# Kernel optimization log

Hardware: AMD Instinct MI355X
Metric: run time of the kernel (lower is better)

## Reference

```python
import jax, jax.numpy as jnp
import numpy as np

B, T, E = 2048, 200, 128
H1, H2 = 64, 32
NEG_INF = -(2.0 ** 32) + 1.0  # matches tf source's -2**32 + 1 padding value


def setup_inputs() -> dict:
    key = jax.random.key(0)
    ks = jax.random.split(key, 8)
    queries = jax.random.normal(ks[0], (B, E), dtype=jnp.float32)
    keys = jax.random.normal(ks[1], (B, T, E), dtype=jnp.float32)
    keys_id = jax.random.randint(ks[2], (B, T), 0, 2, dtype=jnp.int32)
    # Dense params: MLP input is concat([q,k,q-k,q*k]) -> 4*E = 512
    W1 = jax.random.normal(ks[3], (4 * E, H1), dtype=jnp.float32) * (1.0 / np.sqrt(4 * E))
    b1 = jnp.zeros((H1,), dtype=jnp.float32)
    W2 = jax.random.normal(ks[4], (H1, H2), dtype=jnp.float32) * (1.0 / np.sqrt(H1))
    b2 = jnp.zeros((H2,), dtype=jnp.float32)
    W3 = jax.random.normal(ks[5], (H2, 1), dtype=jnp.float32) * (1.0 / np.sqrt(H2))
    b3 = jnp.zeros((1,), dtype=jnp.float32)
    return {"queries": queries, "keys": keys, "keys_id": keys_id,
            "W1": W1, "b1": b1, "W2": W2, "b2": b2, "W3": W3, "b3": b3}


def reference(queries, keys, keys_id, W1, b1, W2, b2, W3, b3):
    # tile query over the time axis: [B,E] -> [B,T,E]
    q = jnp.broadcast_to(queries[:, None, :], keys.shape)
    # concat features: [B,T,4E]
    feat = jnp.concatenate([q, keys, q - keys, q * keys], axis=2)
    # small MLP scorer
    h = jax.nn.relu(jnp.einsum('btf,fh->bth', feat, W1) + b1)
    h = jax.nn.relu(jnp.einsum('bth,hk->btk', h, W2) + b2)
    weight = jnp.einsum('btk,ko->bto', h, W3) + b3  # [B,T,1]
    # masked softmax over time axis (padding id == 0)
    mask = (keys_id != 0)[:, :, None]  # [B,T,1]
    weight = jnp.where(mask, weight, jnp.float32(NEG_INF))
    weight = jax.nn.softmax(weight, axis=1)
    # weighted mean pooling (original uses reduce_mean, i.e. sum/T)
    return jnp.mean(weight * keys, axis=1)  # [B,E]
```

## Files before the change

kernel.cpp:

```cpp
#include <hip/hip_runtime.h>
#include <hip/hip_bf16.h>

#define NEG_INF_F (-4294967295.0f)

typedef __attribute__((ext_vector_type(8))) short bf16x8;
typedef __attribute__((ext_vector_type(4))) float f32x4;

__device__ __forceinline__ unsigned short f2bf(float x) {
    unsigned u = __float_as_uint(x);
    return (unsigned short)((u + 0x7fffu + ((u >> 16) & 1u)) >> 16);
}
__device__ __forceinline__ unsigned f2bf2(float a, float b) {
    __hip_bfloat162 h2 = __float22bfloat162_rn(make_float2(a, b));
    unsigned r; __builtin_memcpy(&r, &h2, 4); return r;
}
union FragU { unsigned u[4]; bf16x8 h; };

struct __align__(16) Smem {
    unsigned short Mt[64 * 128];
    unsigned short h1s[4][16 * 64];
    float q[128];
    float cpart[256];
    float Om[4][128];
    float mw[4], lw[4];
};

__global__ __launch_bounds__(256, 3)
void attn_fused(const float* __restrict__ Q,
                const float* __restrict__ Kg,
                const int*   __restrict__ kid,
                const float* __restrict__ W1,
                const float* __restrict__ b1,
                const float* __restrict__ W2,
                const float* __restrict__ b2,
                const float* __restrict__ W3,
                const float* __restrict__ b3,
                float* __restrict__ out)
{
    __shared__ Smem sm;
    const int b    = blockIdx.x;
    const int tid  = threadIdx.x;
    const int wave = tid >> 6;
    const int lane = tid & 63;
    const int l15  = lane & 15;
    const int quad = lane >> 4;

    if (tid < 128) sm.q[tid] = Q[b * 128 + tid];

    bf16x8 W2f[2][2];
    #pragma unroll
    for (int ks = 0; ks < 2; ++ks) {
        #pragma unroll
        for (int nt = 0; nt < 2; ++nt) {
            const int n = nt * 16 + l15;
            const int kb = ks * 32 + quad * 8;
            bf16x8 f;
            #pragma unroll
            for (int j = 0; j < 8; ++j) f[j] = (short)f2bf(W2[(kb + j) * 32 + n]);
            W2f[ks][nt] = f;
        }
    }
    const float w3a = W3[l15],  w3b = W3[16 + l15];
    const float b2a = b2[l15],  b2b = b2[16 + l15];
    const float b3v = b3[0];
    __syncthreads();

    {
        const int n  = tid & 63;
        const int ko = (tid >> 6) * 2;
        #pragma unroll
        for (int i = 0; i < 16; ++i) {
            const int k = i * 8 + ko;
            const float v0 = (W1[(128 + k) * 64 + n] - W1[(256 + k) * 64 + n])
                           + sm.q[k] * W1[(384 + k) * 64 + n];
            const float v1 = (W1[(129 + k) * 64 + n] - W1[(257 + k) * 64 + n])
                           + sm.q[k + 1] * W1[(385 + k) * 64 + n];
            const int g = (k >> 3) ^ (n & 15);
            *reinterpret_cast<unsigned*>(&sm.Mt[n * 128 + g * 8 + (k & 7)]) = f2bf2(v0, v1);
        }
    }
    {
        const int n = tid & 63, kc = tid >> 6;
        float acc = (kc == 0) ? b1[n] : 0.0f;
        #pragma unroll 4
        for (int i = 0; i < 32; ++i) {
            const int k = kc * 32 + i;
            acc += sm.q[k] * (W1[k * 64 + n] + W1[(256 + k) * 64 + n]);
        }
        sm.cpart[kc * 64 + n] = acc;
    }
    __syncthreads();

    float cn[4];
    #pragma unroll
    for (int nt = 0; nt < 4; ++nt) {
        const int n = nt * 16 + l15;
        cn[nt] = sm.cpart[n] + sm.cpart[64 + n] + sm.cpart[128 + n] + sm.cpart[192 + n];
    }

    const float* kbase = Kg + (size_t)b * 25600;
    unsigned short* h1w = &sm.h1s[wave][0];
    const f32x4 zero4 = {0.f, 0.f, 0.f, 0.f};

    float O[32];
    #pragma unroll
    for (int i = 0; i < 32; ++i) O[i] = 0.0f;
    float mrun = -__builtin_inff(), lrun = 0.0f;

    for (int tile = wave; tile < 13; tile += 4) {
        const int t0 = tile * 16;
        const int t  = t0 + l15;
        const int tr = min(t, 199);
        const float* kr = kbase + tr * 128;
        float4 ka[4], kb_[4];
        #pragma unroll
        for (int ks = 0; ks < 4; ++ks) {
            ka[ks]  = *reinterpret_cast<const float4*>(kr + ks * 32 + quad * 8);
            kb_[ks] = *reinterpret_cast<const float4*>(kr + ks * 32 + quad * 8 + 4);
        }
        const int kidv = kid[b * 200 + tr];

        f32x4 acc[4] = {zero4, zero4, zero4, zero4};
        #pragma unroll
        for (int ks = 0; ks < 4; ++ks) {
            FragU A;
            A.u[0] = f2bf2(ka[ks].x,  ka[ks].y);
            A.u[1] = f2bf2(ka[ks].z,  ka[ks].w);
            A.u[2] = f2bf2(kb_[ks].x, kb_[ks].y);
            A.u[3] = f2bf2(kb_[ks].z, kb_[ks].w);
            #pragma unroll
            for (int nt = 0; nt < 4; ++nt) {
                const int n = nt * 16 + l15;
                const int g = (ks * 4 + quad) ^ l15;
                const bf16x8 Bf = *reinterpret_cast<const bf16x8*>(&sm.Mt[n * 128 + g * 8]);
                acc[nt] = __builtin_amdgcn_mfma_f32_16x16x32_bf16(A.h, Bf, acc[nt], 0, 0, 0);
            }
        }
        #pragma unroll
        for (int nt = 0; nt < 4; ++nt) {
            const int n = nt * 16 + l15;
            #pragma unroll
            for (int r = 0; r < 4; ++r) {
                const int m = quad * 4 + r;
                const float h = fmaxf(acc[nt][r] + cn[nt], 0.0f);
                const int g = (n >> 3) ^ (m & 7);
                h1w[m * 64 + g * 8 + (n & 7)] = f2bf(h);
            }
        }
        f32x4 p0 = zero4, p1 = zero4;
        #pragma unroll
        for (int ks = 0; ks < 2; ++ks) {
            const int g = (ks * 4 + quad) ^ (l15 & 7);
            const bf16x8 A2l = *reinterpret_cast<const bf16x8*>(&h1w[l15 * 64 + g * 8]);
            p0 = __builtin_amdgcn_mfma_f32_16x16x32_bf16(A2l, W2f[ks][0], p0, 0, 0, 0);
            p1 = __builtin_amdgcn_mfma_f32_16x16x32_bf16(A2l, W2f[ks][1], p1, 0, 0, 0);
        }
        float sv[4];
        #pragma unroll
        for (int r = 0; r < 4; ++r)
            sv[r] = fmaxf(p0[r] + b2a, 0.f) * w3a + fmaxf(p1[r] + b2b, 0.f) * w3b;
        #pragma unroll
        for (int off = 1; off < 16; off <<= 1) {
            #pragma unroll
            for (int r = 0; r < 4; ++r) sv[r] += __shfl_xor(sv[r], off);
        }
        const int src = (l15 >> 2) * 16;
        const float s0 = __shfl(sv[0], src), s1 = __shfl(sv[1], src);
        const float s2 = __shfl(sv[2], src), s3 = __shfl(sv[3], src);
        const int rr = l15 & 3;
        const float sres = (rr == 0) ? s0 : (rr == 1) ? s1 : (rr == 2) ? s2 : s3;
        float x;
        if (t < 200) x = (kidv != 0) ? (sres + b3v) : NEG_INF_F;
        else         x = -__builtin_inff();
        float tmax = x;
        #pragma unroll
        for (int off = 1; off < 16; off <<= 1) tmax = fmaxf(tmax, __shfl_xor(tmax, off));
        const float mnew  = fmaxf(mrun, tmax);
        const float alpha = __expf(mrun - mnew);
        const float w     = __expf(x - mnew);
        float tsum = w;
        #pragma unroll
        for (int off = 1; off < 16; off <<= 1) tsum += __shfl_xor(tsum, off);
        lrun = lrun * alpha + tsum;
        mrun = mnew;
        #pragma unroll
        for (int ks = 0; ks < 4; ++ks) {
            O[ks*8+0] = fmaf(O[ks*8+0], alpha, w * ka[ks].x);
            O[ks*8+1] = fmaf(O[ks*8+1], alpha, w * ka[ks].y);
            O[ks*8+2] = fmaf(O[ks*8+2], alpha, w * ka[ks].z);
            O[ks*8+3] = fmaf(O[ks*8+3], alpha, w * ka[ks].w);
            O[ks*8+4] = fmaf(O[ks*8+4], alpha, w * kb_[ks].x);
            O[ks*8+5] = fmaf(O[ks*8+5], alpha, w * kb_[ks].y);
            O[ks*8+6] = fmaf(O[ks*8+6], alpha, w * kb_[ks].z);
            O[ks*8+7] = fmaf(O[ks*8+7], alpha, w * kb_[ks].w);
        }
    }

    #pragma unroll
    for (int off = 1; off < 16; off <<= 1) {
        #pragma unroll
        for (int i = 0; i < 32; ++i) O[i] += __shfl_xor(O[i], off);
    }
    if (l15 == 0) {
        #pragma unroll
        for (int ks = 0; ks < 4; ++ks) {
            *reinterpret_cast<float4*>(&sm.Om[wave][ks * 32 + quad * 8]) =
                make_float4(O[ks*8+0], O[ks*8+1], O[ks*8+2], O[ks*8+3]);
            *reinterpret_cast<float4*>(&sm.Om[wave][ks * 32 + quad * 8 + 4]) =
                make_float4(O[ks*8+4], O[ks*8+5], O[ks*8+6], O[ks*8+7]);
        }
    }
    if (lane == 0) { sm.mw[wave] = mrun; sm.lw[wave] = lrun; }
    __syncthreads();

    if (tid < 128) {
        const float M = fmaxf(fmaxf(sm.mw[0], sm.mw[1]), fmaxf(sm.mw[2], sm.mw[3]));
        float den = 0.f, val = 0.f;
        #pragma unroll
        for (int w = 0; w < 4; ++w) {
            const float a = __expf(sm.mw[w] - M);
            den += sm.lw[w] * a;
            val += sm.Om[w][tid] * a;
        }
        out[(size_t)b * 128 + tid] = val / (den * 200.0f);
    }
}

extern "C" void kernel_launch(void* const* d_in, const int* in_sizes, int n_in,
                              void* d_out, int out_size, void* d_ws, size_t ws_size,
                              hipStream_t stream) {
    (void)in_sizes; (void)n_in; (void)out_size; (void)d_ws; (void)ws_size;
    attn_fused<<<dim3(2048), dim3(256), 0, stream>>>(
        (const float*)d_in[0], (const float*)d_in[1], (const int*)d_in[2],
        (const float*)d_in[3], (const float*)d_in[4], (const float*)d_in[5],
        (const float*)d_in[6], (const float*)d_in[7], (const float*)d_in[8],
        (float*)d_out);
}
```

Measured before the change: 324.1 us.

## Software-pipeline key tile loads with double-buffered register prefetch

Issues the first key tile's global loads at kernel start, before the W1/W2 setup and the query-constant computation, so that latency overlaps the setup. The per-wave tile loop is manually unrolled with two register slots, each tile's loads being prefetched while the previous tile computes. It also packs the h1 bf16 conversions in pairs and skips the online-softmax rescale when the running max does not change. The costs are higher register pressure from the doubled key buffers and more code from the macro-expanded tile bodies.

```diff
diff --git a/kernel.cpp b/kernel.cpp
--- a/kernel.cpp
+++ b/kernel.cpp
@@ -45,6 +45,26 @@
     const int l15  = lane & 15;
     const int quad = lane >> 4;
 
+    const float* kbase   = Kg + (size_t)b * 25600;
+    const int    kidbase = b * 200;
+
+    float4 kA[2][4], kB[2][4];
+    int kidv[2];
+
+#define PREFETCH_K(SLOT, TILE) do {                                             \
+        const int t2_  = (TILE) * 16 + l15;                                     \
+        const int tr2_ = min(t2_, 199);                                         \
+        const float* kr_ = kbase + tr2_ * 128 + quad * 8;                       \
+        _Pragma("unroll")                                                       \
+        for (int ks_ = 0; ks_ < 4; ++ks_) {                                     \
+            kA[SLOT][ks_] = *reinterpret_cast<const float4*>(kr_ + ks_ * 32);   \
+            kB[SLOT][ks_] = *reinterpret_cast<const float4*>(kr_ + ks_ * 32 + 4);\
+        }                                                                       \
+        kidv[SLOT] = kid[kidbase + tr2_];                                       \
+    } while (0)
+
+    PREFETCH_K(0, wave);
+
     if (tid < 128) sm.q[tid] = Q[b * 128 + tid];
 
     bf16x8 W2f[2][2];
@@ -98,7 +118,6 @@
         cn[nt] = sm.cpart[n] + sm.cpart[64 + n] + sm.cpart[128 + n] + sm.cpart[192 + n];
     }
 
-    const float* kbase = Kg + (size_t)b * 25600;
     unsigned short* h1w = &sm.h1s[wave][0];
     const f32x4 zero4 = {0.f, 0.f, 0.f, 0.f};
 
@@ -107,94 +126,120 @@
     for (int i = 0; i < 32; ++i) O[i] = 0.0f;
     float mrun = -__builtin_inff(), lrun = 0.0f;
 
-    for (int tile = wave; tile < 13; tile += 4) {
-        const int t0 = tile * 16;
-        const int t  = t0 + l15;
-        const int tr = min(t, 199);
-        const float* kr = kbase + tr * 128;
-        float4 ka[4], kb_[4];
-        #pragma unroll
-        for (int ks = 0; ks < 4; ++ks) {
-            ka[ks]  = *reinterpret_cast<const float4*>(kr + ks * 32 + quad * 8);
-            kb_[ks] = *reinterpret_cast<const float4*>(kr + ks * 32 + quad * 8 + 4);
-        }
-        const int kidv = kid[b * 200 + tr];
-
-        f32x4 acc[4] = {zero4, zero4, zero4, zero4};
-        #pragma unroll
-        for (int ks = 0; ks < 4; ++ks) {
-            FragU A;
-            A.u[0] = f2bf2(ka[ks].x,  ka[ks].y);
-            A.u[1] = f2bf2(ka[ks].z,  ka[ks].w);
-            A.u[2] = f2bf2(kb_[ks].x, kb_[ks].y);
-            A.u[3] = f2bf2(kb_[ks].z, kb_[ks].w);
-            #pragma unroll
-            for (int nt = 0; nt < 4; ++nt) {
-                const int n = nt * 16 + l15;
-                const int g = (ks * 4 + quad) ^ l15;
-                const bf16x8 Bf = *reinterpret_cast<const bf16x8*>(&sm.Mt[n * 128 + g * 8]);
-                acc[nt] = __builtin_amdgcn_mfma_f32_16x16x32_bf16(A.h, Bf, acc[nt], 0, 0, 0);
-            }
-        }
-        #pragma unroll
-        for (int nt = 0; nt < 4; ++nt) {
-            const int n = nt * 16 + l15;
-            #pragma unroll
-            for (int r = 0; r < 4; ++r) {
-                const int m = quad * 4 + r;
-                const float h = fmaxf(acc[nt][r] + cn[nt], 0.0f);
-                const int g = (n >> 3) ^ (m & 7);
-                h1w[m * 64 + g * 8 + (n & 7)] = f2bf(h);
-            }
-        }
-        f32x4 p0 = zero4, p1 = zero4;
-        #pragma unroll
-        for (int ks = 0; ks < 2; ++ks) {
-            const int g = (ks * 4 + quad) ^ (l15 & 7);
-            const bf16x8 A2l = *reinterpret_cast<const bf16x8*>(&h1w[l15 * 64 + g * 8]);
-            p0 = __builtin_amdgcn_mfma_f32_16x16x32_bf16(A2l, W2f[ks][0], p0, 0, 0, 0);
-            p1 = __builtin_amdgcn_mfma_f32_16x16x32_bf16(A2l, W2f[ks][1], p1, 0, 0, 0);
-        }
-        float sv[4];
-        #pragma unroll
-        for (int r = 0; r < 4; ++r)
-            sv[r] = fmaxf(p0[r] + b2a, 0.f) * w3a + fmaxf(p1[r] + b2b, 0.f) * w3b;
-        #pragma unroll
-        for (int off = 1; off < 16; off <<= 1) {
-            #pragma unroll
-            for (int r = 0; r < 4; ++r) sv[r] += __shfl_xor(sv[r], off);
-        }
-        const int src = (l15 >> 2) * 16;
-        const float s0 = __shfl(sv[0], src), s1 = __shfl(sv[1], src);
-        const float s2 = __shfl(sv[2], src), s3 = __shfl(sv[3], src);
-        const int rr = l15 & 3;
-        const float sres = (rr == 0) ? s0 : (rr == 1) ? s1 : (rr == 2) ? s2 : s3;
-        float x;
-        if (t < 200) x = (kidv != 0) ? (sres + b3v) : NEG_INF_F;
-        else         x = -__builtin_inff();
-        float tmax = x;
-        #pragma unroll
-        for (int off = 1; off < 16; off <<= 1) tmax = fmaxf(tmax, __shfl_xor(tmax, off));
-        const float mnew  = fmaxf(mrun, tmax);
-        const float alpha = __expf(mrun - mnew);
-        const float w     = __expf(x - mnew);
-        float tsum = w;
-        #pragma unroll
-        for (int off = 1; off < 16; off <<= 1) tsum += __shfl_xor(tsum, off);
-        lrun = lrun * alpha + tsum;
-        mrun = mnew;
-        #pragma unroll
-        for (int ks = 0; ks < 4; ++ks) {
-            O[ks*8+0] = fmaf(O[ks*8+0], alpha, w * ka[ks].x);
-            O[ks*8+1] = fmaf(O[ks*8+1], alpha, w * ka[ks].y);
-            O[ks*8+2] = fmaf(O[ks*8+2], alpha, w * ka[ks].z);
-            O[ks*8+3] = fmaf(O[ks*8+3], alpha, w * ka[ks].w);
-            O[ks*8+4] = fmaf(O[ks*8+4], alpha, w * kb_[ks].x);
-            O[ks*8+5] = fmaf(O[ks*8+5], alpha, w * kb_[ks].y);
-            O[ks*8+6] = fmaf(O[ks*8+6], alpha, w * kb_[ks].z);
-            O[ks*8+7] = fmaf(O[ks*8+7], alpha, w * kb_[ks].w);
-        }
-    }
+#define TILE_BODY(CUR, TILE) do {                                               \
+    const int t_ = (TILE) * 16 + l15;                                           \
+    f32x4 acc_[4] = {zero4, zero4, zero4, zero4};                               \
+    _Pragma("unroll")                                                           \
+    for (int ks_ = 0; ks_ < 4; ++ks_) {                                         \
+        FragU A_;                                                               \
+        A_.u[0] = f2bf2(kA[CUR][ks_].x, kA[CUR][ks_].y);                        \
+        A_.u[1] = f2bf2(kA[CUR][ks_].z, kA[CUR][ks_].w);                        \
+        A_.u[2] = f2bf2(kB[CUR][ks_].x, kB[CUR][ks_].y);                        \
+        A_.u[3] = f2bf2(kB[CUR][ks_].z, kB[CUR][ks_].w);                        \
+        const int g_ = (ks_ * 4 + quad) ^ l15;                                  \
+        _Pragma("unroll")                                                       \
+        for (int nt_ = 0; nt_ < 4; ++nt_) {                                     \
+            const bf16x8 Bf_ = *reinterpret_cast<const bf16x8*>(                \
+                &sm.Mt[(nt_ * 16 + l15) * 128 + g_ * 8]);                       \
+            acc_[nt_] = __builtin_amdgcn_mfma_f32_16x16x32_bf16(A_.h, Bf_, acc_[nt_], 0, 0, 0); \
+        }                                                                       \
+    }                                                                           \
+        \
+    const int m0_ = quad * 4;                                                   \
+    _Pragma("unroll")                                                           \
+    for (int nt_ = 0; nt_ < 4; ++nt_) {                                         \
+        const int n_ = nt_ * 16 + l15;                                          \
+        const float h0_ = fmaxf(acc_[nt_][0] + cn[nt_], 0.0f);                  \
+        const float h1_ = fmaxf(acc_[nt_][1] + cn[nt_], 0.0f);                  \
+        const float h2_ = fmaxf(acc_[nt_][2] + cn[nt_], 0.0f);                  \
+        const float h3_ = fmaxf(acc_[nt_][3] + cn[nt_], 0.0f);                  \
+        const unsigned p01_ = f2bf2(h0_, h1_);                                  \
+        const unsigned p23_ = f2bf2(h2_, h3_);                                  \
+        const int nhi_ = n_ >> 3, nlo_ = n_ & 7;                                \
+        h1w[(m0_+0)*64 + ((nhi_ ^ ((m0_+0)&7))*8) + nlo_] = (unsigned short)(p01_);       \
+        h1w[(m0_+1)*64 + ((nhi_ ^ ((m0_+1)&7))*8) + nlo_] = (unsigned short)(p01_ >> 16); \
+        h1w[(m0_+2)*64 + ((nhi_ ^ ((m0_+2)&7))*8) + nlo_] = (unsigned short)(p23_);       \
+        h1w[(m0_+3)*64 + ((nhi_ ^ ((m0_+3)&7))*8) + nlo_] = (unsigned short)(p23_ >> 16); \
+    }                                                                           \
+                                                \
+    f32x4 p0_ = zero4, p1_ = zero4;                                             \
+    _Pragma("unroll")                                                           \
+    for (int ks_ = 0; ks_ < 2; ++ks_) {                                         \
+        const int g_ = (ks_ * 4 + quad) ^ (l15 & 7);                            \
+        const bf16x8 A2_ = *reinterpret_cast<const bf16x8*>(&h1w[l15 * 64 + g_ * 8]); \
+        p0_ = __builtin_amdgcn_mfma_f32_16x16x32_bf16(A2_, W2f[ks_][0], p0_, 0, 0, 0); \
+        p1_ = __builtin_amdgcn_mfma_f32_16x16x32_bf16(A2_, W2f[ks_][1], p1_, 0, 0, 0); \
+    }                                                                           \
+                    \
+    float sv_[4];                                                               \
+    _Pragma("unroll")                                                           \
+    for (int r_ = 0; r_ < 4; ++r_)                                              \
+        sv_[r_] = fmaxf(p0_[r_] + b2a, 0.f) * w3a + fmaxf(p1_[r_] + b2b, 0.f) * w3b; \
+    _Pragma("unroll")                                                           \
+    for (int off_ = 1; off_ < 16; off_ <<= 1) {                                 \
+        _Pragma("unroll")                                                       \
+        for (int r_ = 0; r_ < 4; ++r_) sv_[r_] += __shfl_xor(sv_[r_], off_);    \
+    }                                                                           \
+    const int src_ = (l15 >> 2) * 16;                                           \
+    const float s0_ = __shfl(sv_[0], src_), s1_ = __shfl(sv_[1], src_);         \
+    const float s2_ = __shfl(sv_[2], src_), s3_ = __shfl(sv_[3], src_);         \
+    const int rr_ = l15 & 3;                                                    \
+    const float sres_ = (rr_ == 0) ? s0_ : (rr_ == 1) ? s1_ : (rr_ == 2) ? s2_ : s3_; \
+    float x_;                                                                   \
+    if (t_ < 200) x_ = (kidv[CUR] != 0) ? (sres_ + b3v) : NEG_INF_F;            \
+    else          x_ = -__builtin_inff();                                       \
+    float tmax_ = x_;                                                           \
+    _Pragma("unroll")                                                           \
+    for (int off_ = 1; off_ < 16; off_ <<= 1) tmax_ = fmaxf(tmax_, __shfl_xor(tmax_, off_)); \
+    const float mnew_ = fmaxf(mrun, tmax_);                                     \
+    const float w_ = __expf(x_ - mnew_);                                        \
+    float tsum_ = w_;                                                           \
+    _Pragma("unroll")                                                           \
+    for (int off_ = 1; off_ < 16; off_ <<= 1) tsum_ += __shfl_xor(tsum_, off_); \
+         \
+       \
+       \
+    if (tmax_ > mrun) {                                                         \
+        const float alpha_ = __expf(mrun - mnew_);                              \
+        lrun = fmaf(lrun, alpha_, tsum_);                                       \
+        mrun = mnew_;                                                           \
+        _Pragma("unroll")                                                       \
+        for (int ks_ = 0; ks_ < 4; ++ks_) {                                     \
+            O[ks_*8+0] = fmaf(O[ks_*8+0], alpha_, w_ * kA[CUR][ks_].x);         \
+            O[ks_*8+1] = fmaf(O[ks_*8+1], alpha_, w_ * kA[CUR][ks_].y);         \
+            O[ks_*8+2] = fmaf(O[ks_*8+2], alpha_, w_ * kA[CUR][ks_].z);         \
+            O[ks_*8+3] = fmaf(O[ks_*8+3], alpha_, w_ * kA[CUR][ks_].w);         \
+            O[ks_*8+4] = fmaf(O[ks_*8+4], alpha_, w_ * kB[CUR][ks_].x);         \
+            O[ks_*8+5] = fmaf(O[ks_*8+5], alpha_, w_ * kB[CUR][ks_].y);         \
+            O[ks_*8+6] = fmaf(O[ks_*8+6], alpha_, w_ * kB[CUR][ks_].z);         \
+            O[ks_*8+7] = fmaf(O[ks_*8+7], alpha_, w_ * kB[CUR][ks_].w);         \
+        }                                                                       \
+    } else {                                                                    \
+        lrun += tsum_;                                                          \
+        _Pragma("unroll")                                                       \
+        for (int ks_ = 0; ks_ < 4; ++ks_) {                                     \
+            O[ks_*8+0] = fmaf(w_, kA[CUR][ks_].x, O[ks_*8+0]);                  \
+            O[ks_*8+1] = fmaf(w_, kA[CUR][ks_].y, O[ks_*8+1]);                  \
+            O[ks_*8+2] = fmaf(w_, kA[CUR][ks_].z, O[ks_*8+2]);                  \
+            O[ks_*8+3] = fmaf(w_, kA[CUR][ks_].w, O[ks_*8+3]);                  \
+            O[ks_*8+4] = fmaf(w_, kB[CUR][ks_].x, O[ks_*8+4]);                  \
+            O[ks_*8+5] = fmaf(w_, kB[CUR][ks_].y, O[ks_*8+5]);                  \
+            O[ks_*8+6] = fmaf(w_, kB[CUR][ks_].z, O[ks_*8+6]);                  \
+            O[ks_*8+7] = fmaf(w_, kB[CUR][ks_].w, O[ks_*8+7]);                  \
+        }                                                                       \
+    }                                                                           \
+} while (0)
+
+    PREFETCH_K(1, wave + 4);
+    TILE_BODY(0, wave);
+    PREFETCH_K(0, wave + 8);
+    TILE_BODY(1, wave + 4);
+    if (wave == 0) PREFETCH_K(1, 12);
+    TILE_BODY(0, wave + 8);
+    if (wave == 0) TILE_BODY(1, 12);
+
+#undef TILE_BODY
+#undef PREFETCH_K
 
     #pragma unroll
     for (int off = 1; off < 16; off <<= 1) {
```

After: 355.1 us. +9.6%, slower.
